# Optimization experiments

Measured on AMD Instinct MI355X. Metric: run time of the kernel, lower is better.

The kernel has to match this reference:

```python
import jax, jax.numpy as jnp
import numpy as np

B, L, M, H = 8, 256, 128, 768


def setup_inputs() -> dict:
    key = jax.random.key(0)
    ks = jax.random.split(key, 12)
    s = 1.0 / np.sqrt(H)
    sa = 1.0 / np.sqrt(2 * H)
    return {
        "text_features": jax.random.normal(ks[0], (B, L, H), jnp.float32),
        "dns_features": jax.random.normal(ks[1], (B, M, H), jnp.float32),
        # block 1 params (text_linear_1 has bias, dns_linear_1 no bias, att_linear_1: 2H->1)
        "W_t1": jax.random.uniform(ks[2], (H, H), jnp.float32, -s, s),
        "b_t1": jax.random.uniform(ks[3], (H,), jnp.float32, -s, s),
        "W_d1": jax.random.uniform(ks[4], (H, H), jnp.float32, -s, s),
        "w_att1": jax.random.uniform(ks[5], (2 * H,), jnp.float32, -sa, sa),
        "b_att1": jax.random.uniform(ks[6], (), jnp.float32, -sa, sa),
        # block 2 params (dns_linear_2 has bias, text_linear_2 no bias, att_linear_2: 2H->1)
        "W_d2": jax.random.uniform(ks[7], (H, H), jnp.float32, -s, s),
        "b_d2": jax.random.uniform(ks[8], (H,), jnp.float32, -s, s),
        "W_t2": jax.random.uniform(ks[9], (H, H), jnp.float32, -s, s),
        "w_att2": jax.random.uniform(ks[10], (2 * H,), jnp.float32, -sa, sa),
        "b_att2": jax.random.uniform(ks[11], (), jnp.float32, -sa, sa),
    }


def reference(text_features, dns_features, W_t1, b_t1, W_d1, w_att1, b_att1,
              W_d2, b_d2, W_t2, w_att2, b_att2):
    # Block 1: additive co-attention text -> dns.
    # tanh(cat([Lin(text_rep), Lin(dns_rep)])) @ w_att1 decomposes because tanh is
    # elementwise on the concat and the 2H->1 linear splits into two H-dot-products.
    t1 = jnp.tanh(jnp.einsum('blh,oh->blo', text_features, W_t1) + b_t1)  # (B,L,H)
    d1 = jnp.tanh(jnp.einsum('bmh,oh->bmo', dns_features, W_d1))          # (B,M,H)
    wa, wb = w_att1[:H], w_att1[H:]
    score1 = (t1 @ wa)[:, :, None] + (d1 @ wb)[:, None, :] + b_att1       # (B,L,M)
    a1 = jax.nn.softmax(score1, axis=-1)
    att_dns = jnp.einsum('blm,bmh->blh', a1, dns_features)                # (B,L,H)

    # Block 2: additive co-attention dns-context -> text.
    d2 = jnp.tanh(jnp.einsum('blh,oh->blo', att_dns, W_d2) + b_d2)        # (B,L,H)
    t2 = jnp.tanh(jnp.einsum('bjh,oh->bjo', text_features, W_t2))         # (B,L,H)
    wc, wd = w_att2[:H], w_att2[H:]
    score2 = (d2 @ wc)[:, :, None] + (t2 @ wd)[:, None, :] + b_att2       # (B,L,L)
    a2 = jax.nn.softmax(score2, axis=-1)
    att_text = jnp.einsum('blj,bjh->blh', a2, text_features)              # (B,L,H)

    return (att_text, att_dns)
```

## Files before the change

### kernel.cpp

```cpp
#include <hip/hip_runtime.h>
#include <hip/hip_bf16.h>
#include <math.h>

#define HH 768
#define NB 8
#define LL 256
#define MM 128
#define NROW1 (NB*MM)
#define NROW2 (NB*LL)
#define NROWS (NROW1+NROW2)
#define NCB 12

typedef __attribute__((ext_vector_type(8))) short  bf16x8;
typedef __attribute__((ext_vector_type(4))) float  f32x4;

static __device__ __forceinline__ unsigned int pkbf2(float a, float b) {
    __hip_bfloat162 h = __float22bfloat162_rn(make_float2(a, b));
    unsigned int u; __builtin_memcpy(&u, &h, 4); return u;
}

static __device__ __forceinline__ float fast_tanh(float x) {
    float e = __expf(2.0f * x);
    return 1.0f - 2.0f * __builtin_amdgcn_rcpf(e + 1.0f);
}

__global__ __launch_bounds__(256) void prep_bf16(
    const float4* __restrict__ text, const float4* __restrict__ dns,
    const float4* __restrict__ Wd1, const float4* __restrict__ Wt2,
    uint2* __restrict__ Xb, uint2* __restrict__ Wb)
{
    const int i = blockIdx.x * 256 + threadIdx.x;
    const float4* src; uint2* dst;
    if (i < 589824) {
        dst = Xb + i;
        src = (i < 196608) ? (dns + i) : (text + (i - 196608));
    } else {
        dst = Wb + (i - 589824);
        src = (i < 737280) ? (Wd1 + (i - 589824)) : (Wt2 + (i - 737280));
    }
    float4 v = *src;
    uint2 o; o.x = pkbf2(v.x, v.y); o.y = pkbf2(v.z, v.w);
    *dst = o;
}

__global__ __launch_bounds__(256) void score_mfma(
    const unsigned short* __restrict__ Xb, const unsigned short* __restrict__ Wb,
    const float* __restrict__ wv1, const float* __restrict__ wv2,
    float* __restrict__ partial)
{
    __shared__ __align__(16) unsigned short As[64][72];
    __shared__ __align__(16) unsigned short Bs[64][72];

    const int t = threadIdx.x;
    const int tile = (blockIdx.x >> 3) + (blockIdx.x & 7) * 72;
    const int rb = tile / 12, cb = tile % 12;
    const int row0 = rb * 64, col0 = cb * 64;

    const unsigned short* X = Xb + (size_t)row0 * HH;
    const unsigned short* W; const float* wv;
    if (row0 < NROW1) { W = Wb;                    wv = wv1; }
    else              { W = Wb + (size_t)HH * HH;  wv = wv2; }

    const int sr = t >> 2;
    const int c4 = t & 3;
    const unsigned short* xp = X + (size_t)sr * HH + c4 * 16;
    const unsigned short* wp = W + (size_t)(col0 + sr) * HH + c4 * 16;

    const int l  = t & 63;
    const int w  = t >> 6;
    const int wr = w * 16;
    const int lc = l & 15;
    const int lk = (l >> 4) * 8;

    f32x4 acc[4] = {};
    uint4 rA0, rA1, rB0, rB1, nA0, nA1, nB0, nB1;

    auto STAGE = [&]() {
        *reinterpret_cast<uint4*>(&As[sr][c4 * 16    ]) = rA0;
        *reinterpret_cast<uint4*>(&As[sr][c4 * 16 + 8]) = rA1;
        *reinterpret_cast<uint4*>(&Bs[sr][c4 * 16    ]) = rB0;
        *reinterpret_cast<uint4*>(&Bs[sr][c4 * 16 + 8]) = rB1;
    };
    auto MFMA_TILE = [&]() {
        #pragma unroll
        for (int kk = 0; kk < 2; ++kk) {
            const int ko = kk * 32 + lk;
            bf16x8 a = *reinterpret_cast<const bf16x8*>(&As[wr + lc][ko]);
            #pragma unroll
            for (int n = 0; n < 4; ++n) {
                bf16x8 b = *reinterpret_cast<const bf16x8*>(&Bs[n*16 + lc][ko]);
                acc[n] = __builtin_amdgcn_mfma_f32_16x16x32_bf16(a, b, acc[n], 0, 0, 0);
            }
        }
    };

    rA0 = *(const uint4*)(xp);     rA1 = *(const uint4*)(xp + 8);
    rB0 = *(const uint4*)(wp);     rB1 = *(const uint4*)(wp + 8);

    #pragma unroll 1
    for (int k0 = 0; k0 < HH - 64; k0 += 64) {
        STAGE();
        __syncthreads();
        nA0 = *(const uint4*)(xp + k0 + 64);  nA1 = *(const uint4*)(xp + k0 + 72);
        nB0 = *(const uint4*)(wp + k0 + 64);  nB1 = *(const uint4*)(wp + k0 + 72);
        MFMA_TILE();
        __syncthreads();
        rA0 = nA0; rA1 = nA1; rB0 = nB0; rB1 = nB1;
    }
    STAGE();
    __syncthreads();
    MFMA_TILE();

    float wvn[4];
    #pragma unroll
    for (int n = 0; n < 4; ++n) wvn[n] = wv[col0 + n*16 + lc];
    #pragma unroll
    for (int i = 0; i < 4; ++i) {
        float s = 0.f;
        #pragma unroll
        for (int n = 0; n < 4; ++n) s += fast_tanh(acc[n][i]) * wvn[n];
        s += __shfl_xor(s, 1);
        s += __shfl_xor(s, 2);
        s += __shfl_xor(s, 4);
        s += __shfl_xor(s, 8);
        if (lc == 0)
            partial[(size_t)(row0 + wr + (l >> 4)*4 + i) * NCB + cb] = s;
    }
}

__global__ __launch_bounds__(256) void softmax_kernel(
    const float* __restrict__ partial, float* __restrict__ p1, float* __restrict__ p2)
{
    const int which = blockIdx.x >> 3;
    const int b = blockIdx.x & 7;
    const int n = which ? 256 : 128;
    const int row_base = which ? (NROW1 + b * 256) : (b * 128);
    float* dst = which ? (p2 + b * 256) : (p1 + b * 128);

    const int t = threadIdx.x;
    float v = -INFINITY;
    if (t < n) {
        float vv = 0.f;
        const float* pr = partial + (size_t)(row_base + t) * NCB;
        #pragma unroll
        for (int c = 0; c < NCB; ++c) vv += pr[c];
        v = vv;
    }

    __shared__ float sbuf[4];
    float m = v;
    #pragma unroll
    for (int d = 1; d < 64; d <<= 1) m = fmaxf(m, __shfl_xor(m, d));
    if ((t & 63) == 0) sbuf[t >> 6] = m;
    __syncthreads();
    m = fmaxf(fmaxf(sbuf[0], sbuf[1]), fmaxf(sbuf[2], sbuf[3]));
    __syncthreads();

    float e = (t < n) ? __expf(v - m) : 0.f;
    float s = e;
    #pragma unroll
    for (int d = 1; d < 64; d <<= 1) s += __shfl_xor(s, d);
    if ((t & 63) == 0) sbuf[t >> 6] = s;
    __syncthreads();
    s = sbuf[0] + sbuf[1] + sbuf[2] + sbuf[3];

    if (t < n) dst[t] = e / s;
}

__global__ __launch_bounds__(256) void wsum_kernel(
    const float* __restrict__ text, const float* __restrict__ dns,
    const float* __restrict__ p1, const float* __restrict__ p2,
    float* __restrict__ pvt, float* __restrict__ pvd)
{
    const int b = blockIdx.x, hc = blockIdx.y, rs = blockIdx.z;
    const int t = threadIdx.x;
    const int h = hc * 128 + (t & 127);
    const int sub = t >> 7;

    const int jr0 = rs * 32 + sub * 16;
    float st = 0.f;
    #pragma unroll
    for (int r = 0; r < 16; ++r)
        st = fmaf(p2[b * LL + jr0 + r], text[(size_t)(b * LL + jr0 + r) * HH + h], st);

    const int mr0 = rs * 16 + sub * 8;
    float sd = 0.f;
    #pragma unroll
    for (int r = 0; r < 8; ++r)
        sd = fmaf(p1[b * MM + mr0 + r], dns[(size_t)(b * MM + mr0 + r) * HH + h], sd);

    __shared__ float bt[256], bd[256];
    bt[t] = st; bd[t] = sd;
    __syncthreads();
    if (sub == 0) {
        pvt[(size_t)(rs * NB + b) * HH + h] = bt[t] + bt[t + 128];
        pvd[(size_t)(rs * NB + b) * HH + h] = bd[t] + bd[t + 128];
    }
}

__global__ __launch_bounds__(256) void bcast_reduce(
    const float4* __restrict__ pvt4, const float4* __restrict__ pvd4,
    float4* __restrict__ out)
{
    const int b = blockIdx.x >> 5;
    const int l0 = (blockIdx.x & 31) * 8;
    const int t = threadIdx.x;
    const int H4 = HH / 4;
    const int n4out = NB * LL * H4;

    __shared__ float4 svt[192], svd[192];
    if (t < 192) {
        float4 a = make_float4(0.f, 0.f, 0.f, 0.f);
        float4 c = make_float4(0.f, 0.f, 0.f, 0.f);
        #pragma unroll
        for (int s = 0; s < 8; ++s) {
            float4 u = pvt4[(size_t)(s * NB + b) * H4 + t];
            float4 v = pvd4[(size_t)(s * NB + b) * H4 + t];
            a.x += u.x; a.y += u.y; a.z += u.z; a.w += u.w;
            c.x += v.x; c.y += v.y; c.z += v.z; c.w += v.w;
        }
        svt[t] = a; svd[t] = c;
    }
    __syncthreads();

    #pragma unroll
    for (int i = t; i < 1536; i += 256) {
        const int row = i / 192, h4 = i % 192;
        const int l = l0 + row;
        out[(size_t)(b * LL + l) * H4 + h4] = svt[h4];
        out[n4out + (size_t)(b * LL + l) * H4 + h4] = svd[h4];
    }
}

extern "C" void kernel_launch(void* const* d_in, const int* in_sizes, int n_in,
                              void* d_out, int out_size, void* d_ws, size_t ws_size,
                              hipStream_t stream) {
    const float* text   = (const float*)d_in[0];
    const float* dns    = (const float*)d_in[1];
    const float* W_d1   = (const float*)d_in[4];
    const float* w_att1 = (const float*)d_in[5];
    const float* W_t2   = (const float*)d_in[9];
    const float* w_att2 = (const float*)d_in[10];

    float* ws      = (float*)d_ws;
    float* partial = ws;
    float* p1      = ws + 36864;
    float* p2      = ws + 37888;
    float* pvt     = ws + 39936;
    float* pvd     = ws + 89088;
    unsigned short* Xb = (unsigned short*)(ws + 138240);
    unsigned short* Wb = Xb + (size_t)NROWS * HH;
    float* out     = (float*)d_out;

    prep_bf16<<<3456, 256, 0, stream>>>(
        (const float4*)text, (const float4*)dns, (const float4*)W_d1,
        (const float4*)W_t2, (uint2*)Xb, (uint2*)Wb);
    score_mfma<<<576, 256, 0, stream>>>(
        Xb, Wb, w_att1 + HH, w_att2 + HH, partial);
    softmax_kernel<<<16, 256, 0, stream>>>(partial, p1, p2);
    wsum_kernel<<<dim3(NB, 6, 8), 256, 0, stream>>>(text, dns, p1, p2, pvt, pvd);
    bcast_reduce<<<256, 256, 0, stream>>>(
        (const float4*)pvt, (const float4*)pvd, (float4*)out);
}
```

Before: 33.21 us.

## Use single-wave direct-load 32x32 MFMA scoring and fuse softmax into weighted sum

Rewrites the score GEMM so each block is a single wavefront using 32x32x16 bf16 MFMA, with operands loaded straight from global into registers under double buffering. This removes the LDS staging and block barriers. The softmax kernel is dropped and folded into the weighted-sum kernel, where every block recomputes the softmax from the partial scores. That saves a launch and the p1/p2 round trip, at the cost of redundant softmax work and lower occupancy per block in the GEMM.

```diff
diff --git a/kernel.cpp b/kernel.cpp
--- a/kernel.cpp
+++ b/kernel.cpp
@@ -11,8 +11,8 @@
 #define NROWS (NROW1+NROW2)
 #define NCB 12
 
-typedef __attribute__((ext_vector_type(8))) short  bf16x8;
-typedef __attribute__((ext_vector_type(4))) float  f32x4;
+typedef __attribute__((ext_vector_type(8)))  short bf16x8;
+typedef __attribute__((ext_vector_type(16))) float f32x16;
 
 static __device__ __forceinline__ unsigned int pkbf2(float a, float b) {
     __hip_bfloat162 h = __float22bfloat162_rn(make_float2(a, b));
@@ -43,137 +43,131 @@
     *dst = o;
 }
 
-__global__ __launch_bounds__(256) void score_mfma(
+__global__ __launch_bounds__(64, 2) void score_direct(
     const unsigned short* __restrict__ Xb, const unsigned short* __restrict__ Wb,
     const float* __restrict__ wv1, const float* __restrict__ wv2,
     float* __restrict__ partial)
 {
-    __shared__ __align__(16) unsigned short As[64][72];
-    __shared__ __align__(16) unsigned short Bs[64][72];
-
-    const int t = threadIdx.x;
+    const int l = threadIdx.x;
     const int tile = (blockIdx.x >> 3) + (blockIdx.x & 7) * 72;
     const int rb = tile / 12, cb = tile % 12;
     const int row0 = rb * 64, col0 = cb * 64;
 
-    const unsigned short* X = Xb + (size_t)row0 * HH;
     const unsigned short* W; const float* wv;
-    if (row0 < NROW1) { W = Wb;                    wv = wv1; }
-    else              { W = Wb + (size_t)HH * HH;  wv = wv2; }
-
-    const int sr = t >> 2;
-    const int c4 = t & 3;
-    const unsigned short* xp = X + (size_t)sr * HH + c4 * 16;
-    const unsigned short* wp = W + (size_t)(col0 + sr) * HH + c4 * 16;
-
-    const int l  = t & 63;
-    const int w  = t >> 6;
-    const int wr = w * 16;
-    const int lc = l & 15;
-    const int lk = (l >> 4) * 8;
-
-    f32x4 acc[4] = {};
-    uint4 rA0, rA1, rB0, rB1, nA0, nA1, nB0, nB1;
-
-    auto STAGE = [&]() {
-        *reinterpret_cast<uint4*>(&As[sr][c4 * 16    ]) = rA0;
-        *reinterpret_cast<uint4*>(&As[sr][c4 * 16 + 8]) = rA1;
-        *reinterpret_cast<uint4*>(&Bs[sr][c4 * 16    ]) = rB0;
-        *reinterpret_cast<uint4*>(&Bs[sr][c4 * 16 + 8]) = rB1;
-    };
-    auto MFMA_TILE = [&]() {
-        #pragma unroll
-        for (int kk = 0; kk < 2; ++kk) {
-            const int ko = kk * 32 + lk;
-            bf16x8 a = *reinterpret_cast<const bf16x8*>(&As[wr + lc][ko]);
+    if (row0 < NROW1) { W = Wb;                   wv = wv1; }
+    else              { W = Wb + (size_t)HH * HH; wv = wv2; }
+
+    const int lr = l & 31;
+    const int lk = (l >> 5) * 8;
+    const unsigned short* xp = Xb + (size_t)(row0 + lr) * HH + lk;
+    const unsigned short* wp = W  + (size_t)(col0 + lr) * HH + lk;
+
+    f32x16 acc[2][2] = {};
+    uint4 a0[2][2], b0[2][2], a1[2][2], b1[2][2];
+
+    auto LOAD = [&](uint4 (&a)[2][2], uint4 (&b)[2][2], int k0) {
+        #pragma unroll
+        for (int g = 0; g < 2; ++g) {
             #pragma unroll
-            for (int n = 0; n < 4; ++n) {
-                bf16x8 b = *reinterpret_cast<const bf16x8*>(&Bs[n*16 + lc][ko]);
-                acc[n] = __builtin_amdgcn_mfma_f32_16x16x32_bf16(a, b, acc[n], 0, 0, 0);
+            for (int s = 0; s < 2; ++s) {
+                a[g][s] = *(const uint4*)(xp + (size_t)g * 32 * HH + k0 + s * 16);
+                b[g][s] = *(const uint4*)(wp + (size_t)g * 32 * HH + k0 + s * 16);
             }
         }
     };
-
-    rA0 = *(const uint4*)(xp);     rA1 = *(const uint4*)(xp + 8);
-    rB0 = *(const uint4*)(wp);     rB1 = *(const uint4*)(wp + 8);
-
+    auto MF = [&](uint4 (&a)[2][2], uint4 (&b)[2][2]) {
+        #pragma unroll
+        for (int s = 0; s < 2; ++s)
+            #pragma unroll
+            for (int rg = 0; rg < 2; ++rg)
+                #pragma unroll
+                for (int cg = 0; cg < 2; ++cg)
+                    acc[rg][cg] = __builtin_amdgcn_mfma_f32_32x32x16_bf16(
+                        *(const bf16x8*)&a[rg][s], *(const bf16x8*)&b[cg][s],
+                        acc[rg][cg], 0, 0, 0);
+    };
+
+    LOAD(a0, b0, 0);
     #pragma unroll 1
-    for (int k0 = 0; k0 < HH - 64; k0 += 64) {
-        STAGE();
-        __syncthreads();
-        nA0 = *(const uint4*)(xp + k0 + 64);  nA1 = *(const uint4*)(xp + k0 + 72);
-        nB0 = *(const uint4*)(wp + k0 + 64);  nB1 = *(const uint4*)(wp + k0 + 72);
-        MFMA_TILE();
-        __syncthreads();
-        rA0 = nA0; rA1 = nA1; rB0 = nB0; rB1 = nB1;
-    }
-    STAGE();
-    __syncthreads();
-    MFMA_TILE();
-
-    float wvn[4];
-    #pragma unroll
-    for (int n = 0; n < 4; ++n) wvn[n] = wv[col0 + n*16 + lc];
-    #pragma unroll
-    for (int i = 0; i < 4; ++i) {
-        float s = 0.f;
-        #pragma unroll
-        for (int n = 0; n < 4; ++n) s += fast_tanh(acc[n][i]) * wvn[n];
-        s += __shfl_xor(s, 1);
-        s += __shfl_xor(s, 2);
-        s += __shfl_xor(s, 4);
-        s += __shfl_xor(s, 8);
-        if (lc == 0)
-            partial[(size_t)(row0 + wr + (l >> 4)*4 + i) * NCB + cb] = s;
-    }
-}
-
-__global__ __launch_bounds__(256) void softmax_kernel(
-    const float* __restrict__ partial, float* __restrict__ p1, float* __restrict__ p2)
-{
-    const int which = blockIdx.x >> 3;
-    const int b = blockIdx.x & 7;
-    const int n = which ? 256 : 128;
-    const int row_base = which ? (NROW1 + b * 256) : (b * 128);
-    float* dst = which ? (p2 + b * 256) : (p1 + b * 128);
-
-    const int t = threadIdx.x;
-    float v = -INFINITY;
-    if (t < n) {
-        float vv = 0.f;
-        const float* pr = partial + (size_t)(row_base + t) * NCB;
-        #pragma unroll
-        for (int c = 0; c < NCB; ++c) vv += pr[c];
-        v = vv;
-    }
-
-    __shared__ float sbuf[4];
-    float m = v;
-    #pragma unroll
-    for (int d = 1; d < 64; d <<= 1) m = fmaxf(m, __shfl_xor(m, d));
-    if ((t & 63) == 0) sbuf[t >> 6] = m;
-    __syncthreads();
-    m = fmaxf(fmaxf(sbuf[0], sbuf[1]), fmaxf(sbuf[2], sbuf[3]));
-    __syncthreads();
-
-    float e = (t < n) ? __expf(v - m) : 0.f;
-    float s = e;
-    #pragma unroll
-    for (int d = 1; d < 64; d <<= 1) s += __shfl_xor(s, d);
-    if ((t & 63) == 0) sbuf[t >> 6] = s;
-    __syncthreads();
-    s = sbuf[0] + sbuf[1] + sbuf[2] + sbuf[3];
-
-    if (t < n) dst[t] = e / s;
-}
-
-__global__ __launch_bounds__(256) void wsum_kernel(
+    for (int k0 = 0; k0 < HH; k0 += 64) {
+        LOAD(a1, b1, k0 + 32);
+        MF(a0, b0);
+        if (k0 + 64 < HH) LOAD(a0, b0, k0 + 64);
+        MF(a1, b1);
+    }
+
+    const float wva = wv[col0 + lr];
+    const float wvb = wv[col0 + 32 + lr];
+    #pragma unroll
+    for (int rg = 0; rg < 2; ++rg) {
+        #pragma unroll
+        for (int r = 0; r < 16; ++r) {
+            float v = fast_tanh(acc[rg][0][r]) * wva + fast_tanh(acc[rg][1][r]) * wvb;
+            v += __shfl_xor(v, 1);
+            v += __shfl_xor(v, 2);
+            v += __shfl_xor(v, 4);
+            v += __shfl_xor(v, 8);
+            v += __shfl_xor(v, 16);
+            if (lr == 0) {
+                const int row = row0 + rg * 32 + (r & 3) + 8 * (r >> 2) + 4 * (l >> 5);
+                partial[(size_t)row * NCB + cb] = v;
+            }
+        }
+    }
+}
+
+__global__ __launch_bounds__(256) void wsum_sm(
     const float* __restrict__ text, const float* __restrict__ dns,
-    const float* __restrict__ p1, const float* __restrict__ p2,
-    float* __restrict__ pvt, float* __restrict__ pvd)
+    const float* __restrict__ partial, float* __restrict__ pvt, float* __restrict__ pvd)
 {
     const int b = blockIdx.x, hc = blockIdx.y, rs = blockIdx.z;
     const int t = threadIdx.x;
+    __shared__ float p1s[128], p2s[256], red[8], bt[256], bd[256];
+
+    if (t < 128) {
+        const float* pr = partial + (size_t)(b * MM + t) * NCB;
+        float s = 0.f;
+        #pragma unroll
+        for (int c = 0; c < NCB; ++c) s += pr[c];
+        p1s[t] = s;
+    }
+    {
+        const float* pr = partial + (size_t)(NROW1 + b * LL + t) * NCB;
+        float s = 0.f;
+        #pragma unroll
+        for (int c = 0; c < NCB; ++c) s += pr[c];
+        p2s[t] = s;
+    }
+    __syncthreads();
+
+    float x1 = (t < 128) ? p1s[t] : -1e30f;
+    float m1 = x1;
+    #pragma unroll
+    for (int d = 1; d < 64; d <<= 1) m1 = fmaxf(m1, __shfl_xor(m1, d));
+    if ((t & 63) == 0) red[t >> 6] = m1;
+    float x2 = p2s[t];
+    float m2 = x2;
+    #pragma unroll
+    for (int d = 1; d < 64; d <<= 1) m2 = fmaxf(m2, __shfl_xor(m2, d));
+    if ((t & 63) == 0) red[4 + (t >> 6)] = m2;
+    __syncthreads();
+    m1 = fmaxf(fmaxf(red[0], red[1]), fmaxf(red[2], red[3]));
+    m2 = fmaxf(fmaxf(red[4], red[5]), fmaxf(red[6], red[7]));
+
+    float e1 = (t < 128) ? __expf(x1 - m1) : 0.f;
+    float e2 = __expf(x2 - m2);
+    __syncthreads();
+    float s1 = e1, s2 = e2;
+    #pragma unroll
+    for (int d = 1; d < 64; d <<= 1) { s1 += __shfl_xor(s1, d); s2 += __shfl_xor(s2, d); }
+    if ((t & 63) == 0) { red[t >> 6] = s1; red[4 + (t >> 6)] = s2; }
+    __syncthreads();
+    s1 = red[0] + red[1] + red[2] + red[3];
+    s2 = red[4] + red[5] + red[6] + red[7];
+    if (t < 128) p1s[t] = e1 / s1;
+    p2s[t] = e2 / s2;
+    __syncthreads();
+
     const int h = hc * 128 + (t & 127);
     const int sub = t >> 7;
 
@@ -181,15 +175,14 @@
     float st = 0.f;
     #pragma unroll
     for (int r = 0; r < 16; ++r)
-        st = fmaf(p2[b * LL + jr0 + r], text[(size_t)(b * LL + jr0 + r) * HH + h], st);
+        st = fmaf(p2s[jr0 + r], text[(size_t)(b * LL + jr0 + r) * HH + h], st);
 
     const int mr0 = rs * 16 + sub * 8;
     float sd = 0.f;
     #pragma unroll
     for (int r = 0; r < 8; ++r)
-        sd = fmaf(p1[b * MM + mr0 + r], dns[(size_t)(b * MM + mr0 + r) * HH + h], sd);
-
-    __shared__ float bt[256], bd[256];
+        sd = fmaf(p1s[mr0 + r], dns[(size_t)(b * MM + mr0 + r) * HH + h], sd);
+
     bt[t] = st; bd[t] = sd;
     __syncthreads();
     if (sub == 0) {
@@ -226,9 +219,9 @@
     #pragma unroll
     for (int i = t; i < 1536; i += 256) {
         const int row = i / 192, h4 = i % 192;
-        const int l = l0 + row;
-        out[(size_t)(b * LL + l) * H4 + h4] = svt[h4];
-        out[n4out + (size_t)(b * LL + l) * H4 + h4] = svd[h4];
+        const int ll = l0 + row;
+        out[(size_t)(b * LL + ll) * H4 + h4] = svt[h4];
+        out[n4out + (size_t)(b * LL + ll) * H4 + h4] = svd[h4];
     }
 }
 
@@ -244,21 +237,18 @@
 
     float* ws      = (float*)d_ws;
     float* partial = ws;
-    float* p1      = ws + 36864;
-    float* p2      = ws + 37888;
-    float* pvt     = ws + 39936;
-    float* pvd     = ws + 89088;
-    unsigned short* Xb = (unsigned short*)(ws + 138240);
+    float* pvt     = ws + 36864;
+    float* pvd     = ws + 86016;
+    unsigned short* Xb = (unsigned short*)(ws + 135168);
     unsigned short* Wb = Xb + (size_t)NROWS * HH;
     float* out     = (float*)d_out;
 
     prep_bf16<<<3456, 256, 0, stream>>>(
         (const float4*)text, (const float4*)dns, (const float4*)W_d1,
         (const float4*)W_t2, (uint2*)Xb, (uint2*)Wb);
-    score_mfma<<<576, 256, 0, stream>>>(
+    score_direct<<<576, 64, 0, stream>>>(
         Xb, Wb, w_att1 + HH, w_att2 + HH, partial);
-    softmax_kernel<<<16, 256, 0, stream>>>(partial, p1, p2);
-    wsum_kernel<<<dim3(NB, 6, 8), 256, 0, stream>>>(text, dns, p1, p2, pvt, pvd);
+    wsum_sm<<<dim3(NB, 6, 8), 256, 0, stream>>>(text, dns, partial, pvt, pvd);
     bcast_reduce<<<256, 256, 0, stream>>>(
         (const float4*)pvt, (const float4*)pvd, (float4*)out);
 }
```

Measured after the change: 45.12 us. +35.9%, slower.
